# Optimization experiments

Hardware: AMD Instinct MI355X
Metric: run time of the kernel (lower is better)

Reference implementation:

```python
import jax, jax.numpy as jnp
import numpy as np

T, N, B, D = 64, 8, 128, 128      # time, n_agents, batch, obs_dim
H, S, K, A = 512, 64, 16, 16       # hidden_dim, subtask_dim, num_subtasks, action_dim
NB = N * B


def setup_inputs() -> dict:
    key = jax.random.key(0)
    ks = jax.random.split(key, 16)
    r = lambda i, shape: jax.random.normal(ks[i], shape, jnp.float32) * 0.02
    return dict(
        h1=jnp.zeros((NB, H), jnp.float32),
        h2=jnp.zeros((NB, H), jnp.float32),
        obs=jax.random.normal(ks[0], (T, N, B, D), jnp.float32),
        done=jax.random.bernoulli(ks[1], 0.05, (T, NB)),
        W_embed=r(2, (D, H)), b_embed=jnp.zeros((H,), jnp.float32),
        Wi1=r(3, (H, 3 * H)), bi1=jnp.zeros((3 * H,), jnp.float32),
        Wh1=r(4, (H, 3 * H)), bhn1=jnp.zeros((H,), jnp.float32),
        W_sub=r(5, (H, S)), b_sub=jnp.zeros((S,), jnp.float32),
        W_e1=r(6, (K, S)), b_e1=jnp.zeros((S,), jnp.float32),
        W_e2=r(7, (S, S)), b_e2=jnp.zeros((S,), jnp.float32),
        W_pol=r(8, (D, H)), b_pol=jnp.zeros((H,), jnp.float32),
        Wi2=r(9, (H, 3 * H)), bi2=jnp.zeros((3 * H,), jnp.float32),
        Wh2=r(10, (H, 3 * H)), bhn2=jnp.zeros((H,), jnp.float32),
        W_w1=r(11, (S, H * A)), b_w1=jnp.zeros((H * A,), jnp.float32),
        W_b1=r(12, (S, A)), b_b1=jnp.zeros((A,), jnp.float32),
    )


def _gru(h0, xs, dones, Wi, bi, Wh, bhn):
    """Flax GRUCell with per-step reset-to-zero carry (ScannedRNN)."""
    def step(h, inp):
        x, d = inp
        h = jnp.where(d[:, None], 0.0, h)          # reset carry on done
        gi = x @ Wi + bi                            # (NB, 3H): ir|iz|in
        gh = h @ Wh                                 # (NB, 3H): hr|hz|hn (hn bias separate)
        ir, iz, inn = jnp.split(gi, 3, axis=-1)
        hr, hz, hn = jnp.split(gh, 3, axis=-1)
        rg = jax.nn.sigmoid(ir + hr)
        zg = jax.nn.sigmoid(iz + hz)
        ng = jnp.tanh(inn + rg * (hn + bhn))
        hnew = (1.0 - zg) * ng + zg * h
        return hnew, hnew
    return jax.lax.scan(step, h0, (xs, dones))


def reference(h1, h2, obs, done, W_embed, b_embed, Wi1, bi1, Wh1, bhn1,
              W_sub, b_sub, W_e1, b_e1, W_e2, b_e2, W_pol, b_pol,
              Wi2, bi2, Wh2, bhn2, W_w1, b_w1, W_b1, b_b1):
    t, n, b, _ = obs.shape
    obs_f = obs.reshape(t, n * b, -1)                       # (T, NB, D)

    # agent embedding branch + GRU 1
    ae = jax.nn.relu(obs_f @ W_embed + b_embed)             # (T, NB, H)
    hT1, y1 = _gru(h1, ae, done, Wi1, bi1, Wh1, bhn1)
    ae2 = y1 @ W_sub + b_sub                                # (T, NB, S)
    ae2 = jnp.transpose(ae2.reshape(t, n, b, S), (0, 2, 1, 3))  # (T, B, N, S)

    # subtask embedding: input is eye(K), identical over (t, b) -> compute once
    e = jnp.tanh(jax.nn.relu(jnp.eye(K, dtype=obs.dtype) @ W_e1 + b_e1) @ W_e2 + b_e2)  # (K, S)
    subtask_embed = jnp.broadcast_to(e, (t, b, K, S))

    subtask_logits = jnp.einsum('tbns,ks->tbnk', ae2, e)    # (T, B, N, K)
    subtask_prob = jax.nn.one_hot(jnp.argmax(subtask_logits, axis=-1), K, dtype=obs.dtype)  # eval path

    # subtask policy branch + GRU 2
    sp = jax.nn.relu(obs_f @ W_pol + b_pol)                 # (T, NB, H)
    hT2, y2 = _gru(h2, sp, done, Wi2, bi2, Wh2, bhn2)

    # hypernetwork: _subtask_embed = stop_grad(subtask_embed[:, 0]) == e (time-invariant)
    e_sg = jax.lax.stop_gradient(e)
    w1 = (e_sg @ W_w1 + b_w1).reshape(K, H, A)              # (K, H, A)
    b1 = e_sg @ W_b1 + b_b1                                 # (K, A)

    # equivalent to the repeated-w1 batched matmul, without materializing (T,NB*K,H,A)
    q = jnp.einsum('tbh,kha->tbka', y2, w1) + b1            # (T, NB, K, A), NB in (N,B)-major order

    # faithful to original: prob flattened (B,N)-major vs q flattened (N,B)-major
    prob_flat = subtask_prob.reshape(t, b * n, K)
    q_vals = jnp.einsum('tbk,tbka->tba', prob_flat, q)      # (T, NB, A)

    return ((hT1, hT2), q_vals, subtask_logits, subtask_embed)
```

## Files before the change

kernel.cpp:

```cpp
#include <hip/hip_runtime.h>
#include <hip/hip_bf16.h>
#include <math.h>

#define TT 64
#define NN 8
#define BB 128
#define DD 128
#define HH 512
#define SS 64
#define KK 16
#define AA 16
#define NB 1024
#define H3 (3*HH)

typedef float f4v  __attribute__((ext_vector_type(4)));
typedef float f16v __attribute__((ext_vector_type(16)));
typedef short bf16x8 __attribute__((ext_vector_type(8)));

__device__ __forceinline__ float sigm(float x){ return 1.0f/(1.0f+expf(-x)); }
__device__ __forceinline__ unsigned short f2bf(float f){
  unsigned u = __float_as_uint(f);
  u += 0x7FFF + ((u >> 16) & 1);
  return (unsigned short)(u >> 16);
}
__device__ __forceinline__ float bf2f(unsigned short h){
  return __uint_as_float(((unsigned)h) << 16);
}

__global__ __launch_bounds__(256) void k_detect(const unsigned char* __restrict__ raw,
                                                int* __restrict__ flag)
{
  __shared__ int cA, cB;
  if (threadIdx.x == 0){ cA = 0; cB = 0; }
  __syncthreads();
  int a = 0, b = 0;
  for (int i = threadIdx.x; i < TT*NB; i += 256){
    unsigned char v = raw[i];
    if (v > 1) a++;
    if ((i & 3) != 0 && v != 0) b++;
  }
  atomicAdd(&cA, a); atomicAdd(&cB, b);
  __syncthreads();
  if (threadIdx.x == 0) *flag = (cB == 0) ? 0 : (cA == 0 ? 1 : 2);
}

__global__ __launch_bounds__(256) void k_mask(const unsigned char* __restrict__ raw,
                                              const int* __restrict__ flag,
                                              float* __restrict__ mask)
{
  int i = blockIdx.x*256 + threadIdx.x;
  if (i >= TT*NB) return;
  int f = *flag;
  int v;
  if (f == 1)      v = (int)raw[i];
  else if (f == 0) v = ((const int*)raw)[i];
  else             v = (((const float*)raw)[i] != 0.0f);
  mask[i] = v ? 0.f : 1.f;
}


__global__ __launch_bounds__(256) void k_e(const float* __restrict__ W_e1, const float* __restrict__ b_e1,
                                           const float* __restrict__ W_e2, const float* __restrict__ b_e2,
                                           float* __restrict__ e_out)
{
  __shared__ float r1[KK*SS];
  int tid = threadIdx.x;
  for (int i=0;i<4;++i){ int l = tid + i*256; float v = W_e1[l] + b_e1[l & 63]; r1[l] = v > 0.f ? v : 0.f; }
  __syncthreads();
  for (int i=0;i<4;++i){
    int l = tid + i*256; int k = l >> 6, s = l & 63;
    float acc = b_e2[s];
    #pragma unroll 8
    for (int sp=0; sp<64; ++sp) acc += r1[k*64+sp] * W_e2[sp*64 + s];
    e_out[l] = tanhf(acc);
  }
}

__global__ __launch_bounds__(256) void k_w1b1(const float* __restrict__ e, const float* __restrict__ W_w1,
                                              const float* __restrict__ b_w1, const float* __restrict__ W_b1,
                                              const float* __restrict__ b_b1, float* __restrict__ w1,
                                              float* __restrict__ b1)
{
  __shared__ float es[KK*SS];
  int tid = threadIdx.x;
  for (int i=0;i<4;++i) es[tid + i*256] = e[tid + i*256];
  __syncthreads();
  for (int i=0;i<4;++i){
    int l = blockIdx.x*1024 + tid + i*256;
    int k = l >> 13, m = l & 8191;
    float acc = b_w1[m];
    #pragma unroll 8
    for (int s=0;s<64;++s) acc += es[k*64+s] * W_w1[(size_t)s*8192 + m];
    w1[l] = acc;
  }
  if (blockIdx.x == 0){
    int k = tid >> 4, a = tid & 15;
    float acc = b_b1[a];
    #pragma unroll 8
    for (int s=0;s<64;++s) acc += es[k*64+s] * W_b1[s*16 + a];
    b1[tid] = acc;
  }
}

__global__ __launch_bounds__(256) void k_se(const float* __restrict__ e, float* __restrict__ outse)
{
  __shared__ float4 es[256];
  es[threadIdx.x] = ((const float4*)e)[threadIdx.x];
  __syncthreads();
  const int total4 = TT*BB*KK*SS/4;
  for (int i = blockIdx.x*256 + threadIdx.x; i < total4; i += gridDim.x*256)
    ((float4*)outse)[i] = es[i & 255];
}

__global__ void k_copy(const float* __restrict__ src, float* __restrict__ dst, int n4)
{
  int i = blockIdx.x*blockDim.x + threadIdx.x;
  if (i < n4) ((float4*)dst)[i] = ((const float4*)src)[i];
}

__global__ __launch_bounds__(256) void k_tsplit(const float* __restrict__ W,
                                                unsigned short* __restrict__ WTh,
                                                unsigned short* __restrict__ WTl,
                                                int Kd, int Nc)
{
  __shared__ float t[32][33];
  int n0 = blockIdx.x * 32;
  int k0 = blockIdx.y * 32;
  int c = threadIdx.x & 31, r8 = threadIdx.x >> 5;
  for (int i=0;i<4;++i){
    int r = r8 + i*8;
    t[r][c] = W[(size_t)(k0+r)*Nc + n0 + c];
  }
  __syncthreads();
  for (int i=0;i<4;++i){
    int nr = r8 + i*8;
    float v = t[c][nr];
    unsigned short hi = f2bf(v);
    WTh[(size_t)(n0+nr)*Kd + k0 + c] = hi;
    WTl[(size_t)(n0+nr)*Kd + k0 + c] = f2bf(v - bf2f(hi));
  }
}

__global__ void k_split_cast(const float* __restrict__ src,
                             unsigned short* __restrict__ dh,
                             unsigned short* __restrict__ dl, int n8)
{
  int i = blockIdx.x*blockDim.x + threadIdx.x;
  if (i >= n8) return;
  const float4* s = (const float4*)(src + (size_t)i*8);
  float4 a = s[0], b = s[1];
  float x[8] = {a.x,a.y,a.z,a.w,b.x,b.y,b.z,b.w};
  union { unsigned short u[8]; uint4 v; } ph, pl;
  #pragma unroll
  for (int j=0;j<8;++j){
    unsigned short hi = f2bf(x[j]);
    ph.u[j] = hi;
    pl.u[j] = f2bf(x[j] - bf2f(hi));
  }
  *(uint4*)&dh[(size_t)i*8] = ph.v;
  *(uint4*)&dl[(size_t)i*8] = pl.v;
}

template<int KD, int SPLIT, int NTILE, int RELU, int OUTMODE>
__global__ __launch_bounds__(256) void mfma_gemm(
    const unsigned short* Ah, const unsigned short* Al,
    const unsigned short* Bh, const unsigned short* Bl,
    const float* __restrict__ bias,
    float* C, unsigned short* Chi, unsigned short* Clo, int Nstride)
{
  constexpr int NFC = NTILE/16;
  __shared__ __align__(16) unsigned short AsH[128*40];
  __shared__ __align__(16) unsigned short BsH[NTILE*40];
  __shared__ __align__(16) unsigned short AsL[SPLIT ? 128*40 : 8];
  __shared__ __align__(16) unsigned short BsL[SPLIT ? NTILE*40 : 8];
  int tid = threadIdx.x;
  int w = tid >> 6, l = tid & 63;
  int lr = l & 15, lk = (l >> 4) * 8, lq = l >> 4;
  int rowBase = blockIdx.y * 128, colBase = blockIdx.x * NTILE;
  f4v acc[2][NFC];
  f4v z = {0.f,0.f,0.f,0.f};
  #pragma unroll
  for (int i=0;i<2;++i)
    #pragma unroll
    for (int j=0;j<NFC;++j) acc[i][j] = z;

  for (int k0 = 0; k0 < KD; k0 += 32){
    {
      int r = tid >> 1, half = tid & 1;
      size_t src = (size_t)(rowBase + r)*KD + k0 + half*16;
      bf16x8* dA = (bf16x8*)&AsH[r*40 + half*16];
      dA[0] = *(const bf16x8*)&Ah[src];
      dA[1] = *(const bf16x8*)&Ah[src + 8];
      if (SPLIT){
        bf16x8* dL = (bf16x8*)&AsL[r*40 + half*16];
        dL[0] = *(const bf16x8*)&Al[src];
        dL[1] = *(const bf16x8*)&Al[src + 8];
      }
    }
    if (NTILE == 128){
      int r = tid >> 1, half = tid & 1;
      size_t src = (size_t)(colBase + r)*KD + k0 + half*16;
      bf16x8* dB = (bf16x8*)&BsH[r*40 + half*16];
      dB[0] = *(const bf16x8*)&Bh[src];
      dB[1] = *(const bf16x8*)&Bh[src + 8];
      if (SPLIT){
        bf16x8* dL = (bf16x8*)&BsL[r*40 + half*16];
        dL[0] = *(const bf16x8*)&Bl[src];
        dL[1] = *(const bf16x8*)&Bl[src + 8];
      }
    } else {
      int r = tid >> 2, q = tid & 3;
      size_t src = (size_t)(colBase + r)*KD + k0 + q*8;
      *(bf16x8*)&BsH[r*40 + q*8] = *(const bf16x8*)&Bh[src];
      if (SPLIT)
        *(bf16x8*)&BsL[r*40 + q*8] = *(const bf16x8*)&Bl[src];
    }
    __syncthreads();
    bf16x8 aH0 = *(const bf16x8*)&AsH[(w*32 + lr)*40 + lk];
    bf16x8 aH1 = *(const bf16x8*)&AsH[(w*32 + 16 + lr)*40 + lk];
    bf16x8 aL0, aL1;
    if (SPLIT){
      aL0 = *(const bf16x8*)&AsL[(w*32 + lr)*40 + lk];
      aL1 = *(const bf16x8*)&AsL[(w*32 + 16 + lr)*40 + lk];
    }
    #pragma unroll
    for (int fc=0; fc<NFC; ++fc){
      bf16x8 bH = *(const bf16x8*)&BsH[(fc*16 + lr)*40 + lk];
      acc[0][fc] = __builtin_amdgcn_mfma_f32_16x16x32_bf16(aH0, bH, acc[0][fc], 0,0,0);
      acc[1][fc] = __builtin_amdgcn_mfma_f32_16x16x32_bf16(aH1, bH, acc[1][fc], 0,0,0);
      if (SPLIT){
        bf16x8 bL = *(const bf16x8*)&BsL[(fc*16 + lr)*40 + lk];
        acc[0][fc] = __builtin_amdgcn_mfma_f32_16x16x32_bf16(aH0, bL, acc[0][fc], 0,0,0);
        acc[1][fc] = __builtin_amdgcn_mfma_f32_16x16x32_bf16(aH1, bL, acc[1][fc], 0,0,0);
        acc[0][fc] = __builtin_amdgcn_mfma_f32_16x16x32_bf16(aL0, bH, acc[0][fc], 0,0,0);
        acc[1][fc] = __builtin_amdgcn_mfma_f32_16x16x32_bf16(aL1, bH, acc[1][fc], 0,0,0);
      }
    }
    __syncthreads();
  }
  #pragma unroll
  for (int fr=0; fr<2; ++fr){
    #pragma unroll
    for (int fc=0; fc<NFC; ++fc){
      int col = colBase + fc*16 + lr;
      float bv = bias[col];
      #pragma unroll
      for (int r=0;r<4;++r){
        int row = rowBase + w*32 + fr*16 + lq*4 + r;
        float v = acc[fr][fc][r] + bv;
        if (RELU) v = v > 0.f ? v : 0.f;
        size_t o = (size_t)row*Nstride + col;
        if (OUTMODE == 0) C[o] = v;
        else if (OUTMODE == 1) Chi[o] = f2bf(v);
        else {
          unsigned short hi = f2bf(v);
          Chi[o] = hi;
          Clo[o] = f2bf(v - bf2f(hi));
        }
      }
    }
  }
}

__global__ __launch_bounds__(256) void gru_step_mix3(
    const float* __restrict__ hp1, const float* __restrict__ hp2,
    const float* __restrict__ gi1, const float* __restrict__ gi2,
    const unsigned short* __restrict__ Wh1TH, const unsigned short* __restrict__ Wh1TL,
    const unsigned short* __restrict__ Wh2T,
    const float* __restrict__ bhn1, const float* __restrict__ bhn2,
    const float* __restrict__ mask_t,
    float* __restrict__ ho1, float* __restrict__ ho2,
    unsigned short* __restrict__ y1h, unsigned short* __restrict__ y1l)
{
  __shared__ __align__(16) char smem[40960];
  int bid = blockIdx.x;
  int tid = threadIdx.x;
  int w = tid >> 6, l = tid & 63;
  int rf = w & 1, hc = w >> 1;
  int lc = l & 31, lh = l >> 5;
  int sr = tid >> 2, sg = tid & 3;
  f16v z16 = {0,0,0,0,0,0,0,0,0,0,0,0,0,0,0,0};

  if (bid < 128){
    unsigned short* As = (unsigned short*)smem;
    unsigned short* Bs = (unsigned short*)smem + 64*40;
    int ct = bid & 7, rt = bid >> 3;
    int rowBase = rt << 6, colBase = ct << 6;
    float m_st = mask_t[rowBase + sr];
    f16v acc[3] = {z16, z16, z16};

    float4 pA0, pA1;
    bf16x8 pB[3];
    {
      const float4* s = (const float4*)&hp2[(size_t)(rowBase + sr)*HH + sg*8];
      pA0 = s[0]; pA1 = s[1];
      #pragma unroll
      for (int i=0;i<3;++i){
        int unit = i*256 + tid, brow = unit >> 2, q = unit & 3;
        int g = brow >> 6, c = brow & 63;
        pB[i] = *(const bf16x8*)&Wh2T[(size_t)(g*HH + colBase + c)*HH + q*8];
      }
    }
    for (int k0 = 0; k0 < HH; k0 += 32){
      __syncthreads();
      {
        float x[8] = {pA0.x*m_st,pA0.y*m_st,pA0.z*m_st,pA0.w*m_st,
                      pA1.x*m_st,pA1.y*m_st,pA1.z*m_st,pA1.w*m_st};
        union { unsigned short u[8]; uint4 v; } p;
        #pragma unroll
        for (int j=0;j<8;++j) p.u[j] = f2bf(x[j]);
        *(uint4*)&As[sr*40 + sg*8] = p.v;
        #pragma unroll
        for (int i=0;i<3;++i){
          int unit = i*256 + tid, brow = unit >> 2, q = unit & 3;
          *(bf16x8*)&Bs[brow*40 + q*8] = pB[i];
        }
      }
      __syncthreads();
      if (k0 + 32 < HH){
        const float4* s = (const float4*)&hp2[(size_t)(rowBase + sr)*HH + k0 + 32 + sg*8];
        pA0 = s[0]; pA1 = s[1];
        #pragma unroll
        for (int i=0;i<3;++i){
          int unit = i*256 + tid, brow = unit >> 2, q = unit & 3;
          int g = brow >> 6, c = brow & 63;
          pB[i] = *(const bf16x8*)&Wh2T[(size_t)(g*HH + colBase + c)*HH + k0 + 32 + q*8];
        }
      }
      #pragma unroll
      for (int kc=0;kc<32;kc+=16){
        bf16x8 a = *(const bf16x8*)&As[(rf*32 + lc)*40 + kc + lh*8];
        #pragma unroll
        for (int g=0; g<3; ++g){
          bf16x8 b = *(const bf16x8*)&Bs[(g*64 + hc*32 + lc)*40 + kc + lh*8];
          acc[g] = __builtin_amdgcn_mfma_f32_32x32x16_bf16(a, b, acc[g], 0,0,0);
        }
      }
    }
    int col = colBase + hc*32 + lc;
    float bn = bhn2[col];
    #pragma unroll
    for (int r=0;r<16;++r){
      int row = rowBase + rf*32 + (r&3) + 8*(r>>2) + 4*lh;
      size_t gb = (size_t)row*H3 + col;
      float g_r = __builtin_nontemporal_load(&gi2[gb]);
      float g_z = __builtin_nontemporal_load(&gi2[gb + HH]);
      float g_n = __builtin_nontemporal_load(&gi2[gb + 2*HH]);
      float hv  = hp2[(size_t)row*HH + col] * mask_t[row];
      float rg = sigm(g_r + acc[0][r]);
      float zg = sigm(g_z + acc[1][r]);
      float ng = tanhf(g_n + rg*(acc[2][r] + bn));
      ho2[(size_t)row*HH + col] = (1.f - zg)*ng + zg*hv;
    }
  } else {
    unsigned short* AsH = (unsigned short*)smem;
    unsigned short* AsL = AsH + 64*40;
    unsigned short* BsH = AsL + 64*40;
    unsigned short* BsL = BsH + 192*40;
    int bidp = bid - 128;
    int ct = bidp & 7, rt = bidp >> 3;
    int rowBase = rt << 6, colBase = ct << 6;
    int capk = colBase + hc*32;
    float m_st = mask_t[rowBase + sr];
    f16v acc[3] = {z16, z16, z16};
    float hval[16];

    float4 pA0, pA1;
    bf16x8 pBH[3], pBL[3];
    {
      const float4* s = (const float4*)&hp1[(size_t)(rowBase + sr)*HH + sg*8];
      pA0 = s[0]; pA1 = s[1];
      #pragma unroll
      for (int i=0;i<3;++i){
        int unit = i*256 + tid, brow = unit >> 2, q = unit & 3;
        int g = brow >> 6, c = brow & 63;
        size_t src = (size_t)(g*HH + colBase + c)*HH + q*8;
        pBH[i] = *(const bf16x8*)&Wh1TH[src];
        pBL[i] = *(const bf16x8*)&Wh1TL[src];
      }
    }
    for (int k0 = 0; k0 < HH; k0 += 32){
      __syncthreads();
      {
        float x[8] = {pA0.x*m_st,pA0.y*m_st,pA0.z*m_st,pA0.w*m_st,
                      pA1.x*m_st,pA1.y*m_st,pA1.z*m_st,pA1.w*m_st};
        union { unsigned short u[8]; uint4 v; } ph, pl;
        #pragma unroll
        for (int j=0;j<8;++j){
          unsigned short hi = f2bf(x[j]);
          ph.u[j] = hi;
          pl.u[j] = f2bf(x[j] - bf2f(hi));
        }
        *(uint4*)&AsH[sr*40 + sg*8] = ph.v;
        *(uint4*)&AsL[sr*40 + sg*8] = pl.v;
        #pragma unroll
        for (int i=0;i<3;++i){
          int unit = i*256 + tid, brow = unit >> 2, q = unit & 3;
          *(bf16x8*)&BsH[brow*40 + q*8] = pBH[i];
          *(bf16x8*)&BsL[brow*40 + q*8] = pBL[i];
        }
      }
      __syncthreads();
      if (k0 + 32 < HH){
        const float4* s = (const float4*)&hp1[(size_t)(rowBase + sr)*HH + k0 + 32 + sg*8];
        pA0 = s[0]; pA1 = s[1];
        #pragma unroll
        for (int i=0;i<3;++i){
          int unit = i*256 + tid, brow = unit >> 2, q = unit & 3;
          int g = brow >> 6, c = brow & 63;
          size_t src = (size_t)(g*HH + colBase + c)*HH + k0 + 32 + q*8;
          pBH[i] = *(const bf16x8*)&Wh1TH[src];
          pBL[i] = *(const bf16x8*)&Wh1TL[src];
        }
      }
      if (k0 == capk){
        #pragma unroll
        for (int r=0;r<16;++r){
          int rl = rf*32 + (r&3) + 8*(r>>2) + 4*lh;
          hval[r] = bf2f(AsH[rl*40 + lc]) + bf2f(AsL[rl*40 + lc]);
        }
      }
      #pragma unroll
      for (int kc=0;kc<32;kc+=16){
        bf16x8 aH = *(const bf16x8*)&AsH[(rf*32 + lc)*40 + kc + lh*8];
        bf16x8 aL = *(const bf16x8*)&AsL[(rf*32 + lc)*40 + kc + lh*8];
        #pragma unroll
        for (int g=0; g<3; ++g){
          int brow = (g*64 + hc*32 + lc)*40 + kc + lh*8;
          bf16x8 bH = *(const bf16x8*)&BsH[brow];
          bf16x8 bL = *(const bf16x8*)&BsL[brow];
          acc[g] = __builtin_amdgcn_mfma_f32_32x32x16_bf16(aH, bH, acc[g], 0,0,0);
          acc[g] = __builtin_amdgcn_mfma_f32_32x32x16_bf16(aH, bL, acc[g], 0,0,0);
          acc[g] = __builtin_amdgcn_mfma_f32_32x32x16_bf16(aL, bH, acc[g], 0,0,0);
        }
      }
    }
    int col = colBase + hc*32 + lc;
    float bn = bhn1[col];
    #pragma unroll
    for (int r=0;r<16;++r){
      int row = rowBase + rf*32 + (r&3) + 8*(r>>2) + 4*lh;
      size_t gb = (size_t)row*H3 + col;
      float g_r = __builtin_nontemporal_load(&gi1[gb]);
      float g_z = __builtin_nontemporal_load(&gi1[gb + HH]);
      float g_n = __builtin_nontemporal_load(&gi1[gb + 2*HH]);
      float rg = sigm(g_r + acc[0][r]);
      float zg = sigm(g_z + acc[1][r]);
      float ng = tanhf(g_n + rg*(acc[2][r] + bn));
      float o  = (1.f - zg)*ng + zg*hval[r];
      size_t oo = (size_t)row*HH + col;
      ho1[oo] = o;
      unsigned short hi = f2bf(o);
      __builtin_nontemporal_store(hi, &y1h[oo]);
      __builtin_nontemporal_store(f2bf(o - bf2f(hi)), &y1l[oo]);
    }
  }
}

__global__ __launch_bounds__(256) void k_logits(const float* __restrict__ ae2,
    const float* __restrict__ e, float* __restrict__ out_logits, int* __restrict__ argk, int t0)
{
  __shared__ float es[KK*SS];
  int tid = threadIdx.x;
  for (int i=0;i<4;++i) es[tid + i*256] = e[tid + i*256];
  __syncthreads();
  int g = blockIdx.x*256 + tid;
  int t = t0 + (g >> 10), j = g & 1023;
  const float* arow = &ae2[(size_t)g * SS];
  float a[SS];
  #pragma unroll
  for (int i=0;i<16;++i){ float4 v = ((const float4*)arow)[i]; a[4*i]=v.x; a[4*i+1]=v.y; a[4*i+2]=v.z; a[4*i+3]=v.w; }
  float lg[KK];
  float best = -INFINITY; int bk = 0;
  for (int k=0;k<KK;++k){
    float s2 = 0.f;
    #pragma unroll 8
    for (int s=0;s<SS;++s) s2 += a[s]*es[k*SS+s];
    lg[k] = s2;
    if (s2 > best){ best = s2; bk = k; }
  }
  int n = j >> 7, b = j & 127;
  size_t ob = ((size_t)((t*BB + b)*NN + n)) * KK;
  #pragma unroll
  for (int k4=0;k4<4;++k4)
    *(float4*)&out_logits[ob + k4*4] = make_float4(lg[k4*4],lg[k4*4+1],lg[k4*4+2],lg[k4*4+3]);
  argk[(t*BB + b)*NN + n] = bk;
}

__global__ __launch_bounds__(64) void k_qsel(const float* __restrict__ y2,
    const float* __restrict__ w1, const float* __restrict__ b1,
    const int* __restrict__ argk, float* __restrict__ outq)
{
  __shared__ float yr[HH];
  __shared__ float part[64];
  int bj = blockIdx.x;
  int tid = threadIdx.x;
  const float4* row4 = (const float4*)&y2[(size_t)bj*HH];
  ((float4*)yr)[tid]    = row4[tid];
  ((float4*)yr)[tid+64] = row4[tid+64];
  __syncthreads();
  int k = argk[bj];
  int a = tid & 15, q4 = tid >> 4;
  const float* wp = &w1[(size_t)k*HH*AA + a];
  float s = 0.f;
  int h0 = q4*128;
  #pragma unroll 8
  for (int h=h0; h<h0+128; ++h) s += yr[h]*wp[(size_t)h*AA];
  part[tid] = s;
  __syncthreads();
  if (q4 == 0){
    float v = part[a] + part[a+16] + part[a+32] + part[a+48] + b1[k*AA + a];
    outq[(size_t)bj*AA + a] = v;
  }
}

extern "C" void kernel_launch(void* const* d_in, const int* in_sizes, int n_in,
                              void* d_out, int out_size, void* d_ws, size_t ws_size,
                              hipStream_t stream)
{
  (void)in_sizes; (void)n_in; (void)out_size;
  const float* h1     = (const float*)d_in[0];
  const float* h2     = (const float*)d_in[1];
  const float* obs    = (const float*)d_in[2];
  const unsigned char* done_raw = (const unsigned char*)d_in[3];
  const float* W_embed=(const float*)d_in[4];  const float* b_embed=(const float*)d_in[5];
  const float* Wi1    =(const float*)d_in[6];  const float* bi1    =(const float*)d_in[7];
  const float* Wh1    =(const float*)d_in[8];  const float* bhn1   =(const float*)d_in[9];
  const float* W_sub  =(const float*)d_in[10]; const float* b_sub  =(const float*)d_in[11];
  const float* W_e1   =(const float*)d_in[12]; const float* b_e1   =(const float*)d_in[13];
  const float* W_e2   =(const float*)d_in[14]; const float* b_e2   =(const float*)d_in[15];
  const float* W_pol  =(const float*)d_in[16]; const float* b_pol  =(const float*)d_in[17];
  const float* Wi2    =(const float*)d_in[18]; const float* bi2    =(const float*)d_in[19];
  const float* Wh2    =(const float*)d_in[20]; const float* bhn2   =(const float*)d_in[21];
  const float* W_w1   =(const float*)d_in[22]; const float* b_w1   =(const float*)d_in[23];
  const float* W_b1   =(const float*)d_in[24]; const float* b_b1   =(const float*)d_in[25];

  float* out    = (float*)d_out;
  float* outHT1 = out;
  float* outHT2 = out + (size_t)NB*HH;
  float* outQ   = out + 2ull*NB*HH;
  float* outLG  = outQ + (size_t)TT*NB*AA;
  float* outSE  = outLG + (size_t)TT*BB*NN*KK;

  const size_t fixed_f = 2ull*NB*HH + (size_t)TT*NB + 1024
                       + (size_t)KK*HH*AA + 256 + (size_t)TT*NB + 64
                       + 2ull*DD*HH/2 * 2
                       + 4ull*H3*HH
                       + (size_t)HH*SS;
  const size_t per_t_f = (size_t)NB*(2*HH + 2*H3 + SS)
                       + (size_t)NB*(HH/2 + DD + HH + HH);
  int CH = 64;
  while (CH > 1 && (fixed_f + per_t_f*(size_t)CH)*4 > ws_size) CH >>= 1;

  float* buf1   = (float*)d_ws;
  float* buf2   = buf1   + (size_t)CH*NB*HH;
  float* gbuf1  = buf2   + (size_t)CH*NB*HH;
  float* gbuf2  = gbuf1  + (size_t)CH*NB*H3;
  float* ae2buf = gbuf2  + (size_t)CH*NB*H3;
  float* h_last1= ae2buf + (size_t)CH*NB*SS;
  float* h_last2= h_last1+ (size_t)NB*HH;
  float* maskp  = h_last2+ (size_t)NB*HH;
  float* ws_e   = maskp  + (size_t)TT*NB;
  float* ws_w1  = ws_e   + 1024;
  float* ws_b1  = ws_w1  + (size_t)KK*HH*AA;
  int*   ws_argk= (int*)(ws_b1 + 256);
  int*   ws_flag= (int*)(ws_argk + (size_t)TT*NB);
  unsigned short* buf2bf = (unsigned short*)(ws_flag + 64);
  unsigned short* obs_h  = buf2bf + (size_t)CH*NB*HH;
  unsigned short* obs_l  = obs_h  + (size_t)CH*NB*DD;
  unsigned short* ae_h   = obs_l  + (size_t)CH*NB*DD;
  unsigned short* ae_l   = ae_h   + (size_t)CH*NB*HH;
  unsigned short* y1_h   = ae_l   + (size_t)CH*NB*HH;
  unsigned short* y1_l   = y1_h   + (size_t)CH*NB*HH;
  unsigned short* wembt_h= y1_l   + (size_t)CH*NB*HH;
  unsigned short* wembt_l= wembt_h+ (size_t)HH*DD;
  unsigned short* wpolt_h= wembt_l+ (size_t)HH*DD;
  unsigned short* wpolt_l= wpolt_h+ (size_t)HH*DD;
  unsigned short* wi1t_h = wpolt_l+ (size_t)HH*DD;
  unsigned short* wi1t_l = wi1t_h + (size_t)H3*HH;
  unsigned short* wi2t_h = wi1t_l + (size_t)H3*HH;
  unsigned short* wi2t_l = wi2t_h + (size_t)H3*HH;
  unsigned short* wh1t_h = wi2t_l + (size_t)H3*HH;
  unsigned short* wh1t_l = wh1t_h + (size_t)H3*HH;
  unsigned short* wh2t_h = wh1t_l + (size_t)H3*HH;
  unsigned short* wh2t_l = wh2t_h + (size_t)H3*HH;
  unsigned short* wsubt_h= wh2t_l + (size_t)H3*HH;
  unsigned short* wsubt_l= wsubt_h+ (size_t)SS*HH;

  k_detect<<<1,256,0,stream>>>(done_raw, ws_flag);
  k_mask<<<TT*NB/256,256,0,stream>>>(done_raw, ws_flag, maskp);
  k_e<<<1,256,0,stream>>>(W_e1,b_e1,W_e2,b_e2,ws_e);
  k_w1b1<<<128,256,0,stream>>>(ws_e,W_w1,b_w1,W_b1,b_b1,ws_w1,ws_b1);
  k_se<<<2048,256,0,stream>>>(ws_e,outSE);
  k_tsplit<<<dim3(16,4),256,0,stream>>>(W_embed, wembt_h, wembt_l, DD, HH);
  k_tsplit<<<dim3(16,4),256,0,stream>>>(W_pol,   wpolt_h, wpolt_l, DD, HH);
  k_tsplit<<<dim3(48,16),256,0,stream>>>(Wi1, wi1t_h, wi1t_l, HH, H3);
  k_tsplit<<<dim3(48,16),256,0,stream>>>(Wi2, wi2t_h, wi2t_l, HH, H3);
  k_tsplit<<<dim3(48,16),256,0,stream>>>(Wh1, wh1t_h, wh1t_l, HH, H3);
  k_tsplit<<<dim3(48,16),256,0,stream>>>(Wh2, wh2t_h, wh2t_l, HH, H3);
  k_tsplit<<<dim3(2,16),256,0,stream>>>(W_sub, wsubt_h, wsubt_l, HH, SS);
  k_copy<<<512,256,0,stream>>>(h1, h_last1, NB*HH/4);
  k_copy<<<512,256,0,stream>>>(h2, h_last2, NB*HH/4);

  dim3 thr(256);
  const int NCH = TT / CH;
  for (int c = 0; c < NCH; ++c){
    int t0 = c * CH;
    int M = CH*NB;
    const float* obs_c = obs + (size_t)t0*NB*DD;
    k_split_cast<<<(M*DD/8+255)/256,256,0,stream>>>(obs_c, obs_h, obs_l, M*DD/8);
    mfma_gemm<DD,1,128,1,2><<<dim3(HH/128, M/128),thr,0,stream>>>(
        obs_h, obs_l, wembt_h, wembt_l, b_embed, nullptr, ae_h, ae_l, HH);
    mfma_gemm<HH,1,128,0,0><<<dim3(H3/128, M/128),thr,0,stream>>>(
        ae_h, ae_l, wi1t_h, wi1t_l, bi1, gbuf1, nullptr, nullptr, H3);
    mfma_gemm<DD,0,128,1,1><<<dim3(HH/128, M/128),thr,0,stream>>>(
        obs_h, obs_h, wpolt_h, wpolt_h, b_pol, nullptr, buf2bf, nullptr, HH);
    mfma_gemm<HH,0,128,0,0><<<dim3(H3/128, M/128),thr,0,stream>>>(
        buf2bf, buf2bf, wi2t_h, wi2t_h, bi2, gbuf2, nullptr, nullptr, H3);
    for (int lt = 0; lt < CH; ++lt){
      const float* hp1 = (lt == 0) ? h_last1 : (buf1 + (size_t)(lt-1)*NB*HH);
      const float* hp2 = (lt == 0) ? h_last2 : (buf2 + (size_t)(lt-1)*NB*HH);
      gru_step_mix3<<<256, 256, 0, stream>>>(hp1, hp2,
                                             gbuf1 + (size_t)lt*NB*H3, gbuf2 + (size_t)lt*NB*H3,
                                             wh1t_h, wh1t_l, wh2t_h, bhn1, bhn2,
                                             maskp + (size_t)(t0+lt)*NB,
                                             buf1 + (size_t)lt*NB*HH, buf2 + (size_t)lt*NB*HH,
                                             y1_h + (size_t)lt*NB*HH, y1_l + (size_t)lt*NB*HH);
    }
    k_copy<<<512,256,0,stream>>>(buf1 + (size_t)(CH-1)*NB*HH, h_last1, NB*HH/4);
    k_copy<<<512,256,0,stream>>>(buf2 + (size_t)(CH-1)*NB*HH, h_last2, NB*HH/4);
    mfma_gemm<HH,1,64,0,0><<<dim3(1, M/128),thr,0,stream>>>(
        y1_h, y1_l, wsubt_h, wsubt_l, b_sub, ae2buf, nullptr, nullptr, SS);
    k_logits<<<M/256,256,0,stream>>>(ae2buf, ws_e, outLG, ws_argk, t0);
    k_qsel<<<M,64,0,stream>>>(buf2, ws_w1, ws_b1, ws_argk + (size_t)t0*NB, outQ + (size_t)t0*NB*AA);
  }
  k_copy<<<512,256,0,stream>>>(h_last1, outHT1, NB*HH/4);
  k_copy<<<512,256,0,stream>>>(h_last2, outHT2, NB*HH/4);
}
```

Before: 3.143 ms.

## Keep GRU hidden states in bf16 split form to cut per-step traffic

GRU1's hidden state is now carried only as the bf16 hi/lo pair that feeds the next step's MFMA, so the fp32 ho1 store goes away. GRU2 additionally writes a bf16 copy into double-buffered slots. The step kernel now loads pre-split bf16 A operands and applies the done mask as a select, which removes the per-step float-to-bf16 conversion and halves the A-operand read bytes. The ae buffer reuses y1 storage and the final hidden state is rebuilt by merging hi and lo. This adds bookkeeping for the double-buffered slots and chunk-boundary cases, and the k_logits loop is fully unrolled.

```diff
diff --git a/kernel.cpp b/kernel.cpp
--- a/kernel.cpp
+++ b/kernel.cpp
@@ -116,6 +116,36 @@
 {
   int i = blockIdx.x*blockDim.x + threadIdx.x;
   if (i < n4) ((float4*)dst)[i] = ((const float4*)src)[i];
+}
+
+__global__ void k_merge(const unsigned short* __restrict__ h, const unsigned short* __restrict__ l,
+                        float* __restrict__ o, int n8)
+{
+  int i = blockIdx.x*blockDim.x + threadIdx.x;
+  if (i >= n8) return;
+  uint4 vh = *(const uint4*)&h[(size_t)i*8];
+  uint4 vl = *(const uint4*)&l[(size_t)i*8];
+  const unsigned short* ph = (const unsigned short*)&vh;
+  const unsigned short* pl = (const unsigned short*)&vl;
+  float4 o0, o1;
+  o0.x = bf2f(ph[0])+bf2f(pl[0]); o0.y = bf2f(ph[1])+bf2f(pl[1]);
+  o0.z = bf2f(ph[2])+bf2f(pl[2]); o0.w = bf2f(ph[3])+bf2f(pl[3]);
+  o1.x = bf2f(ph[4])+bf2f(pl[4]); o1.y = bf2f(ph[5])+bf2f(pl[5]);
+  o1.z = bf2f(ph[6])+bf2f(pl[6]); o1.w = bf2f(ph[7])+bf2f(pl[7]);
+  float4* d = (float4*)&o[(size_t)i*8];
+  d[0] = o0; d[1] = o1;
+}
+
+__global__ void k_cast_bf16(const float* __restrict__ src, unsigned short* __restrict__ dst, int n8)
+{
+  int i = blockIdx.x*blockDim.x + threadIdx.x;
+  if (i >= n8) return;
+  const float4* s = (const float4*)(src + (size_t)i*8);
+  float4 a = s[0], b = s[1];
+  union { unsigned short u[8]; uint4 v; } p;
+  p.u[0]=f2bf(a.x); p.u[1]=f2bf(a.y); p.u[2]=f2bf(a.z); p.u[3]=f2bf(a.w);
+  p.u[4]=f2bf(b.x); p.u[5]=f2bf(b.y); p.u[6]=f2bf(b.z); p.u[7]=f2bf(b.w);
+  *(uint4*)&dst[(size_t)i*8] = p.v;
 }
 
 __global__ __launch_bounds__(256) void k_tsplit(const float* __restrict__ W,
@@ -262,14 +292,15 @@
   }
 }
 
-__global__ __launch_bounds__(256) void gru_step_mix3(
-    const float* __restrict__ hp1, const float* __restrict__ hp2,
+__global__ __launch_bounds__(256) void gru_step_mix4(
+    const unsigned short* __restrict__ hp1h, const unsigned short* __restrict__ hp1l,
+    const float* __restrict__ hp2, const unsigned short* __restrict__ hp2b,
     const float* __restrict__ gi1, const float* __restrict__ gi2,
     const unsigned short* __restrict__ Wh1TH, const unsigned short* __restrict__ Wh1TL,
     const unsigned short* __restrict__ Wh2T,
     const float* __restrict__ bhn1, const float* __restrict__ bhn2,
     const float* __restrict__ mask_t,
-    float* __restrict__ ho1, float* __restrict__ ho2,
+    float* __restrict__ ho2, unsigned short* __restrict__ ho2b,
     unsigned short* __restrict__ y1h, unsigned short* __restrict__ y1l)
 {
   __shared__ __align__(16) char smem[40960];
@@ -280,20 +311,20 @@
   int lc = l & 31, lh = l >> 5;
   int sr = tid >> 2, sg = tid & 3;
   f16v z16 = {0,0,0,0,0,0,0,0,0,0,0,0,0,0,0,0};
+  uint4 zero4 = {0,0,0,0};
 
   if (bid < 128){
     unsigned short* As = (unsigned short*)smem;
     unsigned short* Bs = (unsigned short*)smem + 64*40;
     int ct = bid & 7, rt = bid >> 3;
     int rowBase = rt << 6, colBase = ct << 6;
-    float m_st = mask_t[rowBase + sr];
+    bool keep = mask_t[rowBase + sr] != 0.f;
     f16v acc[3] = {z16, z16, z16};
 
-    float4 pA0, pA1;
+    uint4 pA;
     bf16x8 pB[3];
     {
-      const float4* s = (const float4*)&hp2[(size_t)(rowBase + sr)*HH + sg*8];
-      pA0 = s[0]; pA1 = s[1];
+      pA = *(const uint4*)&hp2b[(size_t)(rowBase + sr)*HH + sg*8];
       #pragma unroll
       for (int i=0;i<3;++i){
         int unit = i*256 + tid, brow = unit >> 2, q = unit & 3;
@@ -304,12 +335,7 @@
     for (int k0 = 0; k0 < HH; k0 += 32){
       __syncthreads();
       {
-        float x[8] = {pA0.x*m_st,pA0.y*m_st,pA0.z*m_st,pA0.w*m_st,
-                      pA1.x*m_st,pA1.y*m_st,pA1.z*m_st,pA1.w*m_st};
-        union { unsigned short u[8]; uint4 v; } p;
-        #pragma unroll
-        for (int j=0;j<8;++j) p.u[j] = f2bf(x[j]);
-        *(uint4*)&As[sr*40 + sg*8] = p.v;
+        *(uint4*)&As[sr*40 + sg*8] = keep ? pA : zero4;
         #pragma unroll
         for (int i=0;i<3;++i){
           int unit = i*256 + tid, brow = unit >> 2, q = unit & 3;
@@ -318,8 +344,7 @@
       }
       __syncthreads();
       if (k0 + 32 < HH){
-        const float4* s = (const float4*)&hp2[(size_t)(rowBase + sr)*HH + k0 + 32 + sg*8];
-        pA0 = s[0]; pA1 = s[1];
+        pA = *(const uint4*)&hp2b[(size_t)(rowBase + sr)*HH + k0 + 32 + sg*8];
         #pragma unroll
         for (int i=0;i<3;++i){
           int unit = i*256 + tid, brow = unit >> 2, q = unit & 3;
@@ -350,7 +375,10 @@
       float rg = sigm(g_r + acc[0][r]);
       float zg = sigm(g_z + acc[1][r]);
       float ng = tanhf(g_n + rg*(acc[2][r] + bn));
-      ho2[(size_t)row*HH + col] = (1.f - zg)*ng + zg*hv;
+      float o  = (1.f - zg)*ng + zg*hv;
+      size_t oo = (size_t)row*HH + col;
+      ho2[oo] = o;
+      __builtin_nontemporal_store(f2bf(o), &ho2b[oo]);
     }
   } else {
     unsigned short* AsH = (unsigned short*)smem;
@@ -361,15 +389,16 @@
     int ct = bidp & 7, rt = bidp >> 3;
     int rowBase = rt << 6, colBase = ct << 6;
     int capk = colBase + hc*32;
-    float m_st = mask_t[rowBase + sr];
+    bool keep = mask_t[rowBase + sr] != 0.f;
     f16v acc[3] = {z16, z16, z16};
     float hval[16];
 
-    float4 pA0, pA1;
+    uint4 pAh, pAl;
     bf16x8 pBH[3], pBL[3];
     {
-      const float4* s = (const float4*)&hp1[(size_t)(rowBase + sr)*HH + sg*8];
-      pA0 = s[0]; pA1 = s[1];
+      size_t sA = (size_t)(rowBase + sr)*HH + sg*8;
+      pAh = *(const uint4*)&hp1h[sA];
+      pAl = *(const uint4*)&hp1l[sA];
       #pragma unroll
       for (int i=0;i<3;++i){
         int unit = i*256 + tid, brow = unit >> 2, q = unit & 3;
@@ -382,17 +411,8 @@
     for (int k0 = 0; k0 < HH; k0 += 32){
       __syncthreads();
       {
-        float x[8] = {pA0.x*m_st,pA0.y*m_st,pA0.z*m_st,pA0.w*m_st,
-                      pA1.x*m_st,pA1.y*m_st,pA1.z*m_st,pA1.w*m_st};
-        union { unsigned short u[8]; uint4 v; } ph, pl;
-        #pragma unroll
-        for (int j=0;j<8;++j){
-          unsigned short hi = f2bf(x[j]);
-          ph.u[j] = hi;
-          pl.u[j] = f2bf(x[j] - bf2f(hi));
-        }
-        *(uint4*)&AsH[sr*40 + sg*8] = ph.v;
-        *(uint4*)&AsL[sr*40 + sg*8] = pl.v;
+        *(uint4*)&AsH[sr*40 + sg*8] = keep ? pAh : zero4;
+        *(uint4*)&AsL[sr*40 + sg*8] = keep ? pAl : zero4;
         #pragma unroll
         for (int i=0;i<3;++i){
           int unit = i*256 + tid, brow = unit >> 2, q = unit & 3;
@@ -402,8 +422,9 @@
       }
       __syncthreads();
       if (k0 + 32 < HH){
-        const float4* s = (const float4*)&hp1[(size_t)(rowBase + sr)*HH + k0 + 32 + sg*8];
-        pA0 = s[0]; pA1 = s[1];
+        size_t sA = (size_t)(rowBase + sr)*HH + k0 + 32 + sg*8;
+        pAh = *(const uint4*)&hp1h[sA];
+        pAl = *(const uint4*)&hp1l[sA];
         #pragma unroll
         for (int i=0;i<3;++i){
           int unit = i*256 + tid, brow = unit >> 2, q = unit & 3;
@@ -449,7 +470,6 @@
       float ng = tanhf(g_n + rg*(acc[2][r] + bn));
       float o  = (1.f - zg)*ng + zg*hval[r];
       size_t oo = (size_t)row*HH + col;
-      ho1[oo] = o;
       unsigned short hi = f2bf(o);
       __builtin_nontemporal_store(hi, &y1h[oo]);
       __builtin_nontemporal_store(f2bf(o - bf2f(hi)), &y1l[oo]);
@@ -472,9 +492,10 @@
   for (int i=0;i<16;++i){ float4 v = ((const float4*)arow)[i]; a[4*i]=v.x; a[4*i+1]=v.y; a[4*i+2]=v.z; a[4*i+3]=v.w; }
   float lg[KK];
   float best = -INFINITY; int bk = 0;
+  #pragma unroll
   for (int k=0;k<KK;++k){
     float s2 = 0.f;
-    #pragma unroll 8
+    #pragma unroll
     for (int s=0;s<SS;++s) s2 += a[s]*es[k*SS+s];
     lg[k] = s2;
     if (s2 > best){ best = s2; bk = k; }
@@ -542,24 +563,23 @@
   float* outLG  = outQ + (size_t)TT*NB*AA;
   float* outSE  = outLG + (size_t)TT*BB*NN*KK;
 
-  const size_t fixed_f = 2ull*NB*HH + (size_t)TT*NB + 1024
-                       + (size_t)KK*HH*AA + 256 + (size_t)TT*NB + 64
+  const size_t fixed_f = (size_t)TT*NB  + 1024
+                       + (size_t)KK*HH*AA + 256 + (size_t)TT*NB  + 64
+                       + 2ull*NB*HH/2
+                       + 2ull*NB*HH/2
                        + 2ull*DD*HH/2 * 2
                        + 4ull*H3*HH
                        + (size_t)HH*SS;
-  const size_t per_t_f = (size_t)NB*(2*HH + 2*H3 + SS)
-                       + (size_t)NB*(HH/2 + DD + HH + HH);
+  const size_t per_t_f = (size_t)NB*(HH + 2*H3 + SS)
+                       + (size_t)NB*(HH/2 + DD + HH);
   int CH = 64;
   while (CH > 1 && (fixed_f + per_t_f*(size_t)CH)*4 > ws_size) CH >>= 1;
 
-  float* buf1   = (float*)d_ws;
-  float* buf2   = buf1   + (size_t)CH*NB*HH;
+  float* buf2   = (float*)d_ws;
   float* gbuf1  = buf2   + (size_t)CH*NB*HH;
   float* gbuf2  = gbuf1  + (size_t)CH*NB*H3;
   float* ae2buf = gbuf2  + (size_t)CH*NB*H3;
-  float* h_last1= ae2buf + (size_t)CH*NB*SS;
-  float* h_last2= h_last1+ (size_t)NB*HH;
-  float* maskp  = h_last2+ (size_t)NB*HH;
+  float* maskp  = ae2buf + (size_t)CH*NB*SS;
   float* ws_e   = maskp  + (size_t)TT*NB;
   float* ws_w1  = ws_e   + 1024;
   float* ws_b1  = ws_w1  + (size_t)KK*HH*AA;
@@ -568,11 +588,13 @@
   unsigned short* buf2bf = (unsigned short*)(ws_flag + 64);
   unsigned short* obs_h  = buf2bf + (size_t)CH*NB*HH;
   unsigned short* obs_l  = obs_h  + (size_t)CH*NB*DD;
-  unsigned short* ae_h   = obs_l  + (size_t)CH*NB*DD;
-  unsigned short* ae_l   = ae_h   + (size_t)CH*NB*HH;
-  unsigned short* y1_h   = ae_l   + (size_t)CH*NB*HH;
+  unsigned short* y1_h   = obs_l  + (size_t)CH*NB*DD;
   unsigned short* y1_l   = y1_h   + (size_t)CH*NB*HH;
-  unsigned short* wembt_h= y1_l   + (size_t)CH*NB*HH;
+  unsigned short* hl1h   = y1_l   + (size_t)CH*NB*HH;
+  unsigned short* hl1l   = hl1h   + (size_t)NB*HH;
+  unsigned short* y2b0   = hl1l   + (size_t)NB*HH;
+  unsigned short* y2b1   = y2b0   + (size_t)NB*HH;
+  unsigned short* wembt_h= y2b1   + (size_t)NB*HH;
   unsigned short* wembt_l= wembt_h+ (size_t)HH*DD;
   unsigned short* wpolt_h= wembt_l+ (size_t)HH*DD;
   unsigned short* wpolt_l= wpolt_h+ (size_t)HH*DD;
@@ -586,6 +608,7 @@
   unsigned short* wh2t_l = wh2t_h + (size_t)H3*HH;
   unsigned short* wsubt_h= wh2t_l + (size_t)H3*HH;
   unsigned short* wsubt_l= wsubt_h+ (size_t)SS*HH;
+  unsigned short* y2bslot[2] = { y2b0, y2b1 };
 
   k_detect<<<1,256,0,stream>>>(done_raw, ws_flag);
   k_mask<<<TT*NB/256,256,0,stream>>>(done_raw, ws_flag, maskp);
@@ -599,8 +622,8 @@
   k_tsplit<<<dim3(48,16),256,0,stream>>>(Wh1, wh1t_h, wh1t_l, HH, H3);
   k_tsplit<<<dim3(48,16),256,0,stream>>>(Wh2, wh2t_h, wh2t_l, HH, H3);
   k_tsplit<<<dim3(2,16),256,0,stream>>>(W_sub, wsubt_h, wsubt_l, HH, SS);
-  k_copy<<<512,256,0,stream>>>(h1, h_last1, NB*HH/4);
-  k_copy<<<512,256,0,stream>>>(h2, h_last2, NB*HH/4);
+  k_split_cast<<<NB*HH/8/256,256,0,stream>>>(h1, hl1h, hl1l, NB*HH/8);
+  k_cast_bf16<<<NB*HH/8/256,256,0,stream>>>(h2, y2b1, NB*HH/8);
 
   dim3 thr(256);
   const int NCH = TT / CH;
@@ -610,30 +633,34 @@
     const float* obs_c = obs + (size_t)t0*NB*DD;
     k_split_cast<<<(M*DD/8+255)/256,256,0,stream>>>(obs_c, obs_h, obs_l, M*DD/8);
     mfma_gemm<DD,1,128,1,2><<<dim3(HH/128, M/128),thr,0,stream>>>(
-        obs_h, obs_l, wembt_h, wembt_l, b_embed, nullptr, ae_h, ae_l, HH);
+        obs_h, obs_l, wembt_h, wembt_l, b_embed, nullptr, y1_h, y1_l, HH);
     mfma_gemm<HH,1,128,0,0><<<dim3(H3/128, M/128),thr,0,stream>>>(
-        ae_h, ae_l, wi1t_h, wi1t_l, bi1, gbuf1, nullptr, nullptr, H3);
+        y1_h, y1_l, wi1t_h, wi1t_l, bi1, gbuf1, nullptr, nullptr, H3);
     mfma_gemm<DD,0,128,1,1><<<dim3(HH/128, M/128),thr,0,stream>>>(
         obs_h, obs_h, wpolt_h, wpolt_h, b_pol, nullptr, buf2bf, nullptr, HH);
     mfma_gemm<HH,0,128,0,0><<<dim3(H3/128, M/128),thr,0,stream>>>(
         buf2bf, buf2bf, wi2t_h, wi2t_h, bi2, gbuf2, nullptr, nullptr, H3);
     for (int lt = 0; lt < CH; ++lt){
-      const float* hp1 = (lt == 0) ? h_last1 : (buf1 + (size_t)(lt-1)*NB*HH);
-      const float* hp2 = (lt == 0) ? h_last2 : (buf2 + (size_t)(lt-1)*NB*HH);
-      gru_step_mix3<<<256, 256, 0, stream>>>(hp1, hp2,
+      int gstep = t0 + lt;
+      const unsigned short* hp1h = (lt == 0) ? hl1h : (y1_h + (size_t)(lt-1)*NB*HH);
+      const unsigned short* hp1l = (lt == 0) ? hl1l : (y1_l + (size_t)(lt-1)*NB*HH);
+      const float* hp2 = (c == 0 && lt == 0) ? h2 :
+                         (lt == 0 ? buf2 + (size_t)(CH-1)*NB*HH : buf2 + (size_t)(lt-1)*NB*HH);
+      const unsigned short* hp2b = y2bslot[(gstep+1)&1];
+      gru_step_mix4<<<256, 256, 0, stream>>>(hp1h, hp1l, hp2, hp2b,
                                              gbuf1 + (size_t)lt*NB*H3, gbuf2 + (size_t)lt*NB*H3,
                                              wh1t_h, wh1t_l, wh2t_h, bhn1, bhn2,
-                                             maskp + (size_t)(t0+lt)*NB,
-                                             buf1 + (size_t)lt*NB*HH, buf2 + (size_t)lt*NB*HH,
+                                             maskp + (size_t)gstep*NB,
+                                             buf2 + (size_t)lt*NB*HH, y2bslot[gstep&1],
                                              y1_h + (size_t)lt*NB*HH, y1_l + (size_t)lt*NB*HH);
     }
-    k_copy<<<512,256,0,stream>>>(buf1 + (size_t)(CH-1)*NB*HH, h_last1, NB*HH/4);
-    k_copy<<<512,256,0,stream>>>(buf2 + (size_t)(CH-1)*NB*HH, h_last2, NB*HH/4);
+    k_copy<<<256,256,0,stream>>>((const float*)(y1_h + (size_t)(CH-1)*NB*HH), (float*)hl1h, NB*HH/8);
+    k_copy<<<256,256,0,stream>>>((const float*)(y1_l + (size_t)(CH-1)*NB*HH), (float*)hl1l, NB*HH/8);
     mfma_gemm<HH,1,64,0,0><<<dim3(1, M/128),thr,0,stream>>>(
         y1_h, y1_l, wsubt_h, wsubt_l, b_sub, ae2buf, nullptr, nullptr, SS);
     k_logits<<<M/256,256,0,stream>>>(ae2buf, ws_e, outLG, ws_argk, t0);
     k_qsel<<<M,64,0,stream>>>(buf2, ws_w1, ws_b1, ws_argk + (size_t)t0*NB, outQ + (size_t)t0*NB*AA);
   }
-  k_copy<<<512,256,0,stream>>>(h_last1, outHT1, NB*HH/4);
-  k_copy<<<512,256,0,stream>>>(h_last2, outHT2, NB*HH/4);
-}
+  k_merge<<<NB*HH/8/256,256,0,stream>>>(hl1h, hl1l, outHT1, NB*HH/8);
+  k_copy<<<512,256,0,stream>>>(buf2 + (size_t)(CH-1)*NB*HH, outHT2, NB*HH/4);
+}
```

After: 3.358 ms. 1.07x slower.
